# Optimization experiments

Hardware: AMD Instinct MI355X
Metric: run time of the kernel (lower is better)

The kernel has to match this reference:

```python
import jax, jax.numpy as jnp
import numpy as np

B, S, H = 128, 256, 512


def setup_inputs() -> dict:
    key = jax.random.key(0)
    ks = jax.random.split(key, 20)
    sc = 0.02
    inp = {
        "facts": jax.random.normal(ks[0], (B, S, H), jnp.float32),
        "questions": jax.random.normal(ks[1], (B, 1, H), jnp.float32),
        "prevM": jax.random.normal(ks[2], (B, 1, H), jnp.float32),
        # interaction gate MLP: z1 (4H->H), z2 (H->1)
        "z1_w": jax.random.normal(ks[3], (4 * H, H), jnp.float32) * sc,
        "z1_b": jnp.zeros((H,), jnp.float32),
        "z2_w": jax.random.normal(ks[4], (H, 1), jnp.float32) * sc,
        "z2_b": jnp.zeros((1,), jnp.float32),
        # AttentionGRUCell params (input_size = hidden_size = H)
        "Wr": jax.random.normal(ks[5], (H, H), jnp.float32) * sc,
        "br": jnp.zeros((H,), jnp.float32),
        "Ur": jax.random.normal(ks[6], (H, H), jnp.float32) * sc,
        "bur": jnp.zeros((H,), jnp.float32),
        "W": jax.random.normal(ks[7], (H, H), jnp.float32) * sc,
        "bw": jnp.zeros((H,), jnp.float32),
        "U": jax.random.normal(ks[8], (H, H), jnp.float32) * sc,
        "bu": jnp.zeros((H,), jnp.float32),
        # next memory projection (3H -> H)
        "nm_w": jax.random.normal(ks[9], (3 * H, H), jnp.float32) * sc,
        "nm_b": jnp.zeros((H,), jnp.float32),
    }
    return inp


def _episodic_memory(facts, questions, prevM,
                     z1_w, z1_b, z2_w, z2_b,
                     Wr, br, Ur, bur, W, bw, U, bu,
                     nm_w, nm_b):
    # ---- make_interaction ----
    q = questions  # (B,1,H) broadcasts against (B,S,H)
    m = prevM
    z = jnp.concatenate(
        [facts * q, facts * m, jnp.abs(facts - q), jnp.abs(facts - m)],
        axis=2,
    )  # (B,S,4H)
    g_hidden = jnp.tanh(jnp.einsum("bsf,fh->bsh", z, z1_w) + z1_b)
    G_logits = (jnp.einsum("bsh,ho->bso", g_hidden, z2_w) + z2_b)[..., 0]  # (B,S)
    G = jax.nn.softmax(G_logits, axis=1)  # (B,S)

    # ---- AttentionGRU scan over sentences ----
    pre_r = jnp.einsum("bsh,hk->bsh", facts, Wr) + br  # Wr @ fact, all steps
    pre_h = jnp.einsum("bsh,hk->bsh", facts, W) + bw   # W  @ fact, all steps

    def step(C, xs):
        pr, ph, g = xs  # (B,H), (B,H), (B,)
        r = jax.nn.sigmoid(pr + C @ Ur + bur)
        h_tilda = jnp.tanh(ph + r * (C @ U + bu))
        g = g[:, None]
        return g * h_tilda + (1.0 - g) * C, None

    C0 = jnp.zeros((facts.shape[0], Wr.shape[1]), facts.dtype)
    xs = (jnp.swapaxes(pre_r, 0, 1), jnp.swapaxes(pre_h, 0, 1), G.T)  # lead S
    C, _ = jax.lax.scan(step, C0, xs)  # (B,H)

    # ---- next memory ----
    concat = jnp.concatenate([prevM[:, 0], C, questions[:, 0]], axis=1)  # (B,3H)
    next_mem = jax.nn.relu(concat @ nm_w + nm_b)
    return next_mem[:, None, :]  # (B,1,H)


def reference(facts, questions, prevM, z1_w, z1_b, z2_w, z2_b,
              Wr, br, Ur, bur, W, bw, U, bu, nm_w, nm_b):
    return _episodic_memory(facts, questions, prevM, z1_w, z1_b, z2_w, z2_b,
                            Wr, br, Ur, bur, W, bw, U, bu, nm_w, nm_b)
```

## Files before the change

kernel.cpp:

```cpp
#include <hip/hip_runtime.h>
#include <stdint.h>

#define B_ 128
#define S_ 256
#define H_ 512

typedef __attribute__((ext_vector_type(4))) float f32x4;
typedef __attribute__((ext_vector_type(4))) int i32x4;
typedef __attribute__((ext_vector_type(2))) unsigned int u32x2;
typedef __attribute__((ext_vector_type(8))) __bf16 bf16x8;
typedef unsigned long long u64;

#define OFF_G      0
#define OFF_RSR    131072
#define OFF_RSH    133120
#define OFF_FLG    135168
#define OFF_EX     139264
#define OFF_CBUF   401408
#define OFF_BP     663552
#define OFF_PB     2760704
#define OFF_LOGITS 3809280

__device__ __forceinline__ unsigned short f2bf(float f) {
  unsigned u = __builtin_bit_cast(unsigned, f);
  u += 0x7FFFu + ((u >> 16) & 1u);
  return (unsigned short)(u >> 16);
}
__device__ __forceinline__ float fast_sigmoid(float x) {
  return 1.0f / (1.0f + __expf(-x));
}
__device__ __forceinline__ float fast_tanh(float x) {
  return 1.0f - 2.0f / (__expf(2.0f * x) + 1.0f);
}

__global__ void k_prep_bp(const float* __restrict__ z1w,
                          unsigned short* __restrict__ Bp) {
  int t = blockIdx.x * blockDim.x + threadIdx.x;
  int k = t >> 9, n = t & 511;
  Bp[((k >> 3) * 512 + n) * 8 + (k & 7)] = f2bf(z1w[t]);
}

__global__ void k_prep_pb(const float* __restrict__ Ur,
                          const float* __restrict__ U,
                          unsigned short* __restrict__ PB) {
  int t = blockIdx.x * blockDim.x + threadIdx.x;
  int j = t & 7;
  int l = (t >> 3) & 63;
  int kt = (t >> 9) & 15;
  int jn = (t >> 13) & 1;
  int w = (t >> 14) & 7;
  int mem = t >> 17;
  int k = kt * 32 + ((l >> 4) & 3) * 8 + j;
  int n = mem * 128 + ((w & 3) * 2 + jn) * 16 + (l & 15);
  const float* src = (w >> 2) ? U : Ur;
  PB[t] = f2bf(src[k * 512 + n]);
}

__global__ void k_prep_rs(const float* __restrict__ Wr,
                          const float* __restrict__ W,
                          float* __restrict__ rsr, float* __restrict__ rsh) {
  __shared__ float red[4];
  int h2 = blockIdx.x;
  int t = threadIdx.x;
  const float* M = (h2 >= 512) ? W : Wr;
  int h = h2 & 511;
  float sv = M[h * 512 + t] + M[h * 512 + 256 + t];
#pragma unroll
  for (int mask = 1; mask < 64; mask <<= 1) sv += __shfl_xor(sv, mask, 64);
  if ((t & 63) == 0) red[t >> 6] = sv;
  __syncthreads();
  if (t == 0) {
    float tot = red[0] + red[1] + red[2] + red[3];
    ((h2 >= 512) ? rsh : rsr)[h] = tot;
  }
}

__global__ __launch_bounds__(512, 4) void k_gate(
    const float* __restrict__ facts, const float* __restrict__ questions,
    const float* __restrict__ prevM, const float* __restrict__ z1b,
    const float* __restrict__ z2w, const unsigned short* __restrict__ Bp,
    float* __restrict__ logits) {
  __shared__ float qS[512], mS[512], z1bS[512], z2wS[512];
  __shared__ unsigned short At[64 * 40];
  __shared__ unsigned short Bt[16384];
  __shared__ float lp[64 * 4];
  const int tid = threadIdx.x;
  const int row0 = blockIdx.x * 64;
  const int b = row0 >> 8;
  const int s0 = row0 & 255;
  qS[tid] = questions[b * 512 + tid];
  mS[tid] = prevM[b * 512 + tid];
  z1bS[tid] = z1b[tid];
  z2wS[tid] = z2w[tid];
  const int w = tid >> 6, l = tid & 63;
  const int mgrp = w & 1, ngrp = w >> 1;
  const int lm = l & 15, lk = l >> 4;
  f32x4 acc[2][8];
#pragma unroll
  for (int a = 0; a < 2; ++a)
#pragma unroll
    for (int i = 0; i < 8; ++i) acc[a][i] = (f32x4){0.f, 0.f, 0.f, 0.f};
  const int arow = tid >> 3, ac = tid & 7;
  const float* fbase = facts + ((size_t)(b * 256 + s0 + arow)) * 512 + ac * 4;

  for (int kb = 0; kb < 64; ++kb) {
    __syncthreads();
    {
      const char* gsrc = (const char*)Bp + (size_t)kb * 32768 + w * 4096 + l * 16;
#pragma unroll
      for (int i = 0; i < 4; ++i)
        __builtin_amdgcn_global_load_lds(
            (const __attribute__((address_space(1))) unsigned int*)(gsrc +
                                                                    i * 1024),
            (__attribute__((address_space(3))) unsigned int*)((char*)Bt +
                                                              w * 4096 +
                                                              i * 1024),
            16, 0, 0);
    }
    const int part = kb >> 4;
    const int h0 = (kb & 15) * 32;
    f32x4 fv = *(const f32x4*)(fbase + h0);
    f32x4 ov = (part & 1) ? *(const f32x4*)&mS[h0 + ac * 4]
                          : *(const f32x4*)&qS[h0 + ac * 4];
    float z0, z1, z2, z3;
    if (part < 2) {
      z0 = fv[0] * ov[0]; z1 = fv[1] * ov[1];
      z2 = fv[2] * ov[2]; z3 = fv[3] * ov[3];
    } else {
      z0 = fabsf(fv[0] - ov[0]); z1 = fabsf(fv[1] - ov[1]);
      z2 = fabsf(fv[2] - ov[2]); z3 = fabsf(fv[3] - ov[3]);
    }
    unsigned p0 = (unsigned)f2bf(z0) | ((unsigned)f2bf(z1) << 16);
    unsigned p1 = (unsigned)f2bf(z2) | ((unsigned)f2bf(z3) << 16);
    u32x2 pk = {p0, p1};
    *(u32x2*)&At[arow * 40 + ac * 4] = pk;
    __syncthreads();
    bf16x8 af[2];
#pragma unroll
    for (int mi = 0; mi < 2; ++mi) {
      i32x4 av = *(const i32x4*)&At[((mgrp * 2 + mi) * 16 + lm) * 40 + lk * 8];
      af[mi] = __builtin_bit_cast(bf16x8, av);
    }
#pragma unroll
    for (int i = 0; i < 8; ++i) {
      const int nt = ngrp * 8 + i;
      i32x4 bv = *(const i32x4*)&Bt[lk * 4096 + (nt * 16 + lm) * 8];
      bf16x8 bf = __builtin_bit_cast(bf16x8, bv);
      acc[0][i] = __builtin_amdgcn_mfma_f32_16x16x32_bf16(af[0], bf, acc[0][i], 0, 0, 0);
      acc[1][i] = __builtin_amdgcn_mfma_f32_16x16x32_bf16(af[1], bf, acc[1][i], 0, 0, 0);
    }
  }
  float pr_[2][4];
#pragma unroll
  for (int mi = 0; mi < 2; ++mi)
#pragma unroll
    for (int r = 0; r < 4; ++r) pr_[mi][r] = 0.f;
#pragma unroll
  for (int i = 0; i < 8; ++i) {
    const int n_i = (ngrp * 8 + i) * 16 + lm;
    const float zb = z1bS[n_i], zw = z2wS[n_i];
#pragma unroll
    for (int mi = 0; mi < 2; ++mi)
#pragma unroll
      for (int r = 0; r < 4; ++r)
        pr_[mi][r] += fast_tanh(acc[mi][i][r] + zb) * zw;
  }
#pragma unroll
  for (int mask = 1; mask < 16; mask <<= 1)
#pragma unroll
    for (int mi = 0; mi < 2; ++mi)
#pragma unroll
      for (int r = 0; r < 4; ++r)
        pr_[mi][r] += __shfl_xor(pr_[mi][r], mask, 64);
  if (lm == 0) {
#pragma unroll
    for (int mi = 0; mi < 2; ++mi)
#pragma unroll
      for (int r = 0; r < 4; ++r)
        lp[((mgrp * 2 + mi) * 16 + lk * 4 + r) * 4 + ngrp] = pr_[mi][r];
  }
  __syncthreads();
  if (tid < 64)
    logits[row0 + tid] =
        lp[tid * 4] + lp[tid * 4 + 1] + lp[tid * 4 + 2] + lp[tid * 4 + 3];
}

__global__ void k_softmax(const float* __restrict__ logits,
                          float* __restrict__ G) {
  __shared__ float red[4], red2[4];
  int b = blockIdx.x, t = threadIdx.x;
  float v = logits[b * 256 + t];
  float mx = v;
#pragma unroll
  for (int mask = 1; mask < 64; mask <<= 1)
    mx = fmaxf(mx, __shfl_xor(mx, mask, 64));
  if ((t & 63) == 0) red[t >> 6] = mx;
  __syncthreads();
  mx = fmaxf(fmaxf(red[0], red[1]), fmaxf(red[2], red[3]));
  float e = __expf(v - mx);
  float sm = e;
#pragma unroll
  for (int mask = 1; mask < 64; mask <<= 1) sm += __shfl_xor(sm, mask, 64);
  if ((t & 63) == 0) red2[t >> 6] = sm;
  __syncthreads();
  sm = red2[0] + red2[1] + red2[2] + red2[3];
  G[b * 256 + t] = e / sm;
}

__global__ __launch_bounds__(512, 1) void k_scan(
    const float* __restrict__ facts, const float* __restrict__ Gm,
    const unsigned short* __restrict__ PB, const float* __restrict__ rsr,
    const float* __restrict__ rsh, const float* __restrict__ br,
    const float* __restrict__ bur, const float* __restrict__ bw,
    const float* __restrict__ bu, u64* __restrict__ EXq,
    unsigned int* __restrict__ FLG, float* __restrict__ Cb) {
  __shared__ unsigned short A[16 * 520];
  __shared__ float outb[16 * 272];
  const int tid = threadIdx.x;
  const int g = blockIdx.x & 7;
  const int mem = blockIdx.x >> 3;
  const int w = tid >> 6, l = tid & 63;
  const int lm = l & 15, lk = (l >> 4) & 3;
  for (int i = tid; i < 16 * 520 / 4; i += 512) ((u64*)A)[i] = 0ull;
  i32x4 bfr[2][16];
  const char* pb = (const char*)PB + (size_t)(mem * 8 + w) * 32768;
#pragma unroll
  for (int jn = 0; jn < 2; ++jn)
#pragma unroll
    for (int kt = 0; kt < 16; ++kt)
      bfr[jn][kt] = *(const i32x4*)(pb + (jn * 16 + kt) * 1024 + l * 16);
  const int ot = (w >> 2) * 8 + (w & 3) * 2;
  const int bb = tid >> 5;
  const int nqq = tid & 31;
  const int n0 = mem * 128 + nqq * 4;
  const int nl0 = nqq * 4;
  const int batch = g * 16 + bb;
  const f32x4 c_rsr = *(const f32x4*)(rsr + n0);
  const f32x4 c_br  = *(const f32x4*)(br + n0);
  const f32x4 c_rsh = *(const f32x4*)(rsh + n0);
  const f32x4 c_bw  = *(const f32x4*)(bw + n0);
  const f32x4 c_bur = *(const f32x4*)(bur + n0);
  const f32x4 c_bu  = *(const f32x4*)(bu + n0);
  const float* fptr = facts + (size_t)batch * 256 * 512 + n0;
  const float* gptr = Gm + batch * 256;
  const int grow = tid >> 5, gcu = tid & 31;
  const int pollmem = (tid < mem) ? tid : tid + 1;
  f32x4 Cv = (f32x4){0.f, 0.f, 0.f, 0.f};
  __syncthreads();

  for (int s = 0; s < 256; ++s) {
    const unsigned tag = (unsigned)(s + 1);
    const unsigned rbase = ((unsigned)(s & 1) * 8 + (unsigned)g) * 16;
    f32x4 fct = *(const f32x4*)(fptr + (size_t)s * 512);
    float gval = gptr[s];
    f32x4 acc0 = (f32x4){0.f, 0.f, 0.f, 0.f};
    f32x4 acc1 = (f32x4){0.f, 0.f, 0.f, 0.f};
#pragma unroll
    for (int kt = 0; kt < 16; ++kt) {
      i32x4 av = *(const i32x4*)&A[lm * 520 + kt * 32 + lk * 8];
      bf16x8 afv = __builtin_bit_cast(bf16x8, av);
      acc0 = __builtin_amdgcn_mfma_f32_16x16x32_bf16(
          afv, __builtin_bit_cast(bf16x8, bfr[0][kt]), acc0, 0, 0, 0);
      acc1 = __builtin_amdgcn_mfma_f32_16x16x32_bf16(
          afv, __builtin_bit_cast(bf16x8, bfr[1][kt]), acc1, 0, 0, 0);
    }
#pragma unroll
    for (int r = 0; r < 4; ++r) {
      outb[ot * 272 + (lk * 4 + r) * 17 + lm] = acc0[r];
      outb[(ot + 1) * 272 + (lk * 4 + r) * 17 + lm] = acc1[r];
    }
    __syncthreads();
    {
      unsigned short pk[4];
#pragma unroll
      for (int r = 0; r < 4; ++r) {
        const int n_loc = nl0 + r;
        const float uro = outb[(n_loc >> 4) * 272 + bb * 17 + (n_loc & 15)];
        const float uuo =
            outb[(8 + (n_loc >> 4)) * 272 + bb * 17 + (n_loc & 15)];
        const float pr = fct[r] * c_rsr[r] + c_br[r];
        const float ph = fct[r] * c_rsh[r] + c_bw[r];
        const float r_ = fast_sigmoid(pr + uro + c_bur[r]);
        const float ht = fast_tanh(ph + r_ * (uuo + c_bu[r]));
        Cv[r] = gval * ht + (1.0f - gval) * Cv[r];
        pk[r] = f2bf(Cv[r]);
      }
      const u64 word = (u64)pk[0] | ((u64)pk[1] << 16) | ((u64)pk[2] << 32) |
                       ((u64)pk[3] << 48);
      __hip_atomic_store(EXq + (rbase + (unsigned)bb) * 128 + (unsigned)(n0 >> 2),
                         word, __ATOMIC_RELAXED, __HIP_MEMORY_SCOPE_AGENT);
      *(u64*)((char*)A + bb * 1040 + n0 * 2) = word;
    }
    __syncthreads();
    if (tid == 0)
      __hip_atomic_store(FLG + g * 4 + mem, tag, __ATOMIC_RELAXED,
                         __HIP_MEMORY_SCOPE_AGENT);
    if (tid < 3) {
      int guard = 0;
      for (;;) {
        unsigned v = __hip_atomic_load(FLG + g * 4 + pollmem, __ATOMIC_RELAXED,
                                       __HIP_MEMORY_SCOPE_AGENT);
        if (v >= tag) break;
        __builtin_amdgcn_s_sleep(1);
        if (++guard > (1 << 22)) break;
      }
    }
    __syncthreads();
#pragma unroll
    for (int q = 0; q < 4; ++q) {
      if (q != mem) {
        u64 wv = __hip_atomic_load(
            EXq + (rbase + (unsigned)grow) * 128 + (unsigned)(q * 32 + gcu),
            __ATOMIC_RELAXED, __HIP_MEMORY_SCOPE_AGENT);
        *(u64*)((char*)A + grow * 1040 + q * 256 + gcu * 8) = wv;
      }
    }
    __syncthreads();
  }
  *(f32x4*)(Cb + (size_t)batch * 512 + n0) = Cv;
}

__global__ __launch_bounds__(512) void k_final(
    const float* __restrict__ prevM, const float* __restrict__ questions,
    const float* __restrict__ Cb, const float* __restrict__ nmw,
    const float* __restrict__ nmb, float* __restrict__ out) {
  __shared__ float cc[2][1536];
  const int t = threadIdx.x;
  const int b0 = blockIdx.x * 2;
  for (int i = t; i < 1536; i += 512) {
#pragma unroll
    for (int bi = 0; bi < 2; ++bi) {
      int bbx = b0 + bi;
      float v;
      if (i < 512) v = prevM[bbx * 512 + i];
      else if (i < 1024) v = Cb[bbx * 512 + i - 512];
      else v = questions[bbx * 512 + i - 1024];
      cc[bi][i] = v;
    }
  }
  __syncthreads();
  const int h = t;
  float a0 = nmb[h], a1 = nmb[h];
#pragma unroll 4
  for (int f = 0; f < 1536; ++f) {
    float wv = nmw[f * 512 + h];
    a0 = fmaf(cc[0][f], wv, a0);
    a1 = fmaf(cc[1][f], wv, a1);
  }
  out[(size_t)b0 * 512 + h] = fmaxf(a0, 0.f);
  out[(size_t)(b0 + 1) * 512 + h] = fmaxf(a1, 0.f);
}

extern "C" void kernel_launch(void* const* d_in, const int* in_sizes, int n_in,
                              void* d_out, int out_size, void* d_ws,
                              size_t ws_size, hipStream_t stream) {
  const float* facts     = (const float*)d_in[0];
  const float* questions = (const float*)d_in[1];
  const float* prevM     = (const float*)d_in[2];
  const float* z1w       = (const float*)d_in[3];
  const float* z1b       = (const float*)d_in[4];
  const float* z2w       = (const float*)d_in[5];
  const float* Wr        = (const float*)d_in[7];
  const float* br        = (const float*)d_in[8];
  const float* Ur        = (const float*)d_in[9];
  const float* bur       = (const float*)d_in[10];
  const float* W         = (const float*)d_in[11];
  const float* bw        = (const float*)d_in[12];
  const float* U         = (const float*)d_in[13];
  const float* bu        = (const float*)d_in[14];
  const float* nmw       = (const float*)d_in[15];
  const float* nmb       = (const float*)d_in[16];

  char* ws = (char*)d_ws;
  float* G             = (float*)(ws + OFF_G);
  float* rsr           = (float*)(ws + OFF_RSR);
  float* rsh           = (float*)(ws + OFF_RSH);
  unsigned* FLG        = (unsigned*)(ws + OFF_FLG);
  u64* EXq             = (u64*)(ws + OFF_EX);
  float* Cb            = (float*)(ws + OFF_CBUF);
  float* logits        = (float*)(ws + OFF_LOGITS);
  unsigned short* Bp   = (unsigned short*)(ws + OFF_BP);
  unsigned short* PB   = (unsigned short*)(ws + OFF_PB);

  hipMemsetAsync(FLG, 0, 32 * sizeof(unsigned), stream);
  k_prep_bp<<<2048, 512, 0, stream>>>(z1w, Bp);
  k_prep_pb<<<1024, 512, 0, stream>>>(Ur, U, PB);
  k_prep_rs<<<1024, 256, 0, stream>>>(Wr, W, rsr, rsh);
  k_gate<<<512, 512, 0, stream>>>(facts, questions, prevM, z1b, z2w, Bp, logits);
  k_softmax<<<128, 256, 0, stream>>>(logits, G);
  k_scan<<<32, 512, 0, stream>>>(facts, G, PB, rsr, rsh, br, bur, bw, bu, EXq,
                                 FLG, Cb);
  k_final<<<64, 512, 0, stream>>>(prevM, questions, Cb, nmw, nmb, (float*)d_out);
}
```

Before: 1.140 ms.

## Compute GRU gates directly in MFMA accumulator layout and prefetch next-step inputs

Reorders the packed Ur/U weight layout so each wave's two MFMA accumulators hold the Ur and U products for the same 16 output columns. The gate math can then run directly on accumulator registers, removing the LDS round-trip through outb and one barrier per step. Facts and gate values for the next step are prefetched during the current step, using a transposed G written by softmax. Flag polling is spread across all threads, and the exchange loads are batched. The cost is more scattered 4-byte global stores of packed bf16 pairs built with shuffles.

```diff
diff --git a/kernel.cpp b/kernel.cpp
--- a/kernel.cpp
+++ b/kernel.cpp
@@ -47,12 +47,12 @@
   int j = t & 7;
   int l = (t >> 3) & 63;
   int kt = (t >> 9) & 15;
-  int jn = (t >> 13) & 1;
+  int mat = (t >> 13) & 1;
   int w = (t >> 14) & 7;
   int mem = t >> 17;
   int k = kt * 32 + ((l >> 4) & 3) * 8 + j;
-  int n = mem * 128 + ((w & 3) * 2 + jn) * 16 + (l & 15);
-  const float* src = (w >> 2) ? U : Ur;
+  int n = mem * 128 + w * 16 + (l & 15);
+  const float* src = mat ? U : Ur;
   PB[t] = f2bf(src[k * 512 + n]);
 }
 
@@ -186,7 +186,7 @@
 }
 
 __global__ void k_softmax(const float* __restrict__ logits,
-                          float* __restrict__ G) {
+                          float* __restrict__ GT) {
   __shared__ float red[4], red2[4];
   int b = blockIdx.x, t = threadIdx.x;
   float v = logits[b * 256 + t];
@@ -204,18 +204,17 @@
   if ((t & 63) == 0) red2[t >> 6] = sm;
   __syncthreads();
   sm = red2[0] + red2[1] + red2[2] + red2[3];
-  G[b * 256 + t] = e / sm;
+  GT[t * 128 + b] = e / sm;
 }
 
 __global__ __launch_bounds__(512, 1) void k_scan(
-    const float* __restrict__ facts, const float* __restrict__ Gm,
+    const float* __restrict__ facts, const float* __restrict__ GT,
     const unsigned short* __restrict__ PB, const float* __restrict__ rsr,
     const float* __restrict__ rsh, const float* __restrict__ br,
     const float* __restrict__ bur, const float* __restrict__ bw,
-    const float* __restrict__ bu, u64* __restrict__ EXq,
+    const float* __restrict__ bu, unsigned int* __restrict__ EX,
     unsigned int* __restrict__ FLG, float* __restrict__ Cb) {
   __shared__ unsigned short A[16 * 520];
-  __shared__ float outb[16 * 272];
   const int tid = threadIdx.x;
   const int g = blockIdx.x & 7;
   const int mem = blockIdx.x >> 3;
@@ -225,34 +224,31 @@
   i32x4 bfr[2][16];
   const char* pb = (const char*)PB + (size_t)(mem * 8 + w) * 32768;
 #pragma unroll
-  for (int jn = 0; jn < 2; ++jn)
+  for (int mat = 0; mat < 2; ++mat)
 #pragma unroll
     for (int kt = 0; kt < 16; ++kt)
-      bfr[jn][kt] = *(const i32x4*)(pb + (jn * 16 + kt) * 1024 + l * 16);
-  const int ot = (w >> 2) * 8 + (w & 3) * 2;
-  const int bb = tid >> 5;
-  const int nqq = tid & 31;
-  const int n0 = mem * 128 + nqq * 4;
-  const int nl0 = nqq * 4;
-  const int batch = g * 16 + bb;
-  const f32x4 c_rsr = *(const f32x4*)(rsr + n0);
-  const f32x4 c_br  = *(const f32x4*)(br + n0);
-  const f32x4 c_rsh = *(const f32x4*)(rsh + n0);
-  const f32x4 c_bw  = *(const f32x4*)(bw + n0);
-  const f32x4 c_bur = *(const f32x4*)(bur + n0);
-  const f32x4 c_bu  = *(const f32x4*)(bu + n0);
-  const float* fptr = facts + (size_t)batch * 256 * 512 + n0;
-  const float* gptr = Gm + batch * 256;
+      bfr[mat][kt] = *(const i32x4*)(pb + (mat * 16 + kt) * 1024 + l * 16);
+  const int n = mem * 128 + w * 16 + lm;
+  const int b0 = g * 16 + lk * 4;
+  const float c_rsr = rsr[n], c_br = br[n];
+  const float c_rsh = rsh[n], c_bw = bw[n];
+  const float c_bur = bur[n], c_bu = bu[n];
+  const float* fb[4];
+#pragma unroll
+  for (int r = 0; r < 4; ++r)
+    fb[r] = facts + (size_t)(b0 + r) * (256 * 512) + n;
   const int grow = tid >> 5, gcu = tid & 31;
-  const int pollmem = (tid < mem) ? tid : tid + 1;
+  const u64* EXQ = (const u64*)EX;
   f32x4 Cv = (f32x4){0.f, 0.f, 0.f, 0.f};
+  float fct[4];
+#pragma unroll
+  for (int r = 0; r < 4; ++r) fct[r] = fb[r][0];
+  f32x4 gvv = *(const f32x4*)(GT + b0);
   __syncthreads();
 
   for (int s = 0; s < 256; ++s) {
     const unsigned tag = (unsigned)(s + 1);
     const unsigned rbase = ((unsigned)(s & 1) * 8 + (unsigned)g) * 16;
-    f32x4 fct = *(const f32x4*)(fptr + (size_t)s * 512);
-    float gval = gptr[s];
     f32x4 acc0 = (f32x4){0.f, 0.f, 0.f, 0.f};
     f32x4 acc1 = (f32x4){0.f, 0.f, 0.f, 0.f};
 #pragma unroll
@@ -264,60 +260,75 @@
       acc1 = __builtin_amdgcn_mfma_f32_16x16x32_bf16(
           afv, __builtin_bit_cast(bf16x8, bfr[1][kt]), acc1, 0, 0, 0);
     }
+    unsigned pkd[4];
 #pragma unroll
     for (int r = 0; r < 4; ++r) {
-      outb[ot * 272 + (lk * 4 + r) * 17 + lm] = acc0[r];
-      outb[(ot + 1) * 272 + (lk * 4 + r) * 17 + lm] = acc1[r];
-    }
-    __syncthreads();
-    {
-      unsigned short pk[4];
-#pragma unroll
-      for (int r = 0; r < 4; ++r) {
-        const int n_loc = nl0 + r;
-        const float uro = outb[(n_loc >> 4) * 272 + bb * 17 + (n_loc & 15)];
-        const float uuo =
-            outb[(8 + (n_loc >> 4)) * 272 + bb * 17 + (n_loc & 15)];
-        const float pr = fct[r] * c_rsr[r] + c_br[r];
-        const float ph = fct[r] * c_rsh[r] + c_bw[r];
-        const float r_ = fast_sigmoid(pr + uro + c_bur[r]);
-        const float ht = fast_tanh(ph + r_ * (uuo + c_bu[r]));
-        Cv[r] = gval * ht + (1.0f - gval) * Cv[r];
-        pk[r] = f2bf(Cv[r]);
-      }
-      const u64 word = (u64)pk[0] | ((u64)pk[1] << 16) | ((u64)pk[2] << 32) |
-                       ((u64)pk[3] << 48);
-      __hip_atomic_store(EXq + (rbase + (unsigned)bb) * 128 + (unsigned)(n0 >> 2),
-                         word, __ATOMIC_RELAXED, __HIP_MEMORY_SCOPE_AGENT);
-      *(u64*)((char*)A + bb * 1040 + n0 * 2) = word;
+      const float pr = fct[r] * c_rsr + c_br;
+      const float ph = fct[r] * c_rsh + c_bw;
+      const float r_ = fast_sigmoid(pr + acc0[r] + c_bur);
+      const float ht = fast_tanh(ph + r_ * (acc1[r] + c_bu));
+      Cv[r] = gvv[r] * ht + (1.0f - gvv[r]) * Cv[r];
+      const int mb = (int)f2bf(Cv[r]);
+      pkd[r] = (unsigned)mb | ((unsigned)__shfl_xor(mb, 1, 64) << 16);
+    }
+    if (!(lm & 1)) {
+#pragma unroll
+      for (int r = 0; r < 4; ++r)
+        __hip_atomic_store(EX + (rbase + (unsigned)(lk * 4 + r)) * 256 +
+                               ((unsigned)n >> 1),
+                           pkd[r], __ATOMIC_RELAXED, __HIP_MEMORY_SCOPE_AGENT);
+    }
+    float fctn[4];
+    f32x4 gvn = gvv;
+    if (s < 255) {
+#pragma unroll
+      for (int r = 0; r < 4; ++r) fctn[r] = fb[r][(size_t)(s + 1) * 512];
+      gvn = *(const f32x4*)(GT + (s + 1) * 128 + b0);
+    } else {
+#pragma unroll
+      for (int r = 0; r < 4; ++r) fctn[r] = 0.f;
     }
     __syncthreads();
     if (tid == 0)
       __hip_atomic_store(FLG + g * 4 + mem, tag, __ATOMIC_RELAXED,
                          __HIP_MEMORY_SCOPE_AGENT);
-    if (tid < 3) {
-      int guard = 0;
-      for (;;) {
-        unsigned v = __hip_atomic_load(FLG + g * 4 + pollmem, __ATOMIC_RELAXED,
-                                       __HIP_MEMORY_SCOPE_AGENT);
-        if (v >= tag) break;
-        __builtin_amdgcn_s_sleep(1);
-        if (++guard > (1 << 22)) break;
+    if (!(lm & 1)) {
+#pragma unroll
+      for (int r = 0; r < 4; ++r)
+        *(unsigned*)((char*)A + (lk * 4 + r) * 1040 + n * 2) = pkd[r];
+    }
+    {
+#pragma unroll
+      for (int j = 0; j < 3; ++j) {
+        const int q = j + (j >= mem ? 1 : 0);
+        int guard = 0;
+        while (__hip_atomic_load(FLG + g * 4 + q, __ATOMIC_RELAXED,
+                                 __HIP_MEMORY_SCOPE_AGENT) < tag) {
+          __builtin_amdgcn_s_sleep(1);
+          if (++guard > (1 << 22)) break;
+        }
       }
+      u64 wv[3];
+#pragma unroll
+      for (int j = 0; j < 3; ++j) {
+        const int q = j + (j >= mem ? 1 : 0);
+        wv[j] = __hip_atomic_load(
+            EXQ + (rbase + (unsigned)grow) * 128 + (unsigned)(q * 32 + gcu),
+            __ATOMIC_RELAXED, __HIP_MEMORY_SCOPE_AGENT);
+      }
+#pragma unroll
+      for (int j = 0; j < 3; ++j) {
+        const int q = j + (j >= mem ? 1 : 0);
+        *(u64*)((char*)A + grow * 1040 + q * 256 + gcu * 8) = wv[j];
+      }
     }
     __syncthreads();
 #pragma unroll
-    for (int q = 0; q < 4; ++q) {
-      if (q != mem) {
-        u64 wv = __hip_atomic_load(
-            EXq + (rbase + (unsigned)grow) * 128 + (unsigned)(q * 32 + gcu),
-            __ATOMIC_RELAXED, __HIP_MEMORY_SCOPE_AGENT);
-        *(u64*)((char*)A + grow * 1040 + q * 256 + gcu * 8) = wv;
-      }
-    }
-    __syncthreads();
-  }
-  *(f32x4*)(Cb + (size_t)batch * 512 + n0) = Cv;
+    for (int r = 0; r < 4; ++r) fct[r] = fctn[r];
+    gvv = gvn;
+  }
+#pragma unroll
+  for (int r = 0; r < 4; ++r) Cb[(size_t)(b0 + r) * 512 + n] = Cv[r];
 }
 
 __global__ __launch_bounds__(512) void k_final(
@@ -372,11 +383,11 @@
   const float* nmb       = (const float*)d_in[16];
 
   char* ws = (char*)d_ws;
-  float* G             = (float*)(ws + OFF_G);
+  float* GT            = (float*)(ws + OFF_G);
   float* rsr           = (float*)(ws + OFF_RSR);
   float* rsh           = (float*)(ws + OFF_RSH);
   unsigned* FLG        = (unsigned*)(ws + OFF_FLG);
-  u64* EXq             = (u64*)(ws + OFF_EX);
+  unsigned* EX         = (unsigned*)(ws + OFF_EX);
   float* Cb            = (float*)(ws + OFF_CBUF);
   float* logits        = (float*)(ws + OFF_LOGITS);
   unsigned short* Bp   = (unsigned short*)(ws + OFF_BP);
@@ -387,8 +398,8 @@
   k_prep_pb<<<1024, 512, 0, stream>>>(Ur, U, PB);
   k_prep_rs<<<1024, 256, 0, stream>>>(Wr, W, rsr, rsh);
   k_gate<<<512, 512, 0, stream>>>(facts, questions, prevM, z1b, z2w, Bp, logits);
-  k_softmax<<<128, 256, 0, stream>>>(logits, G);
-  k_scan<<<32, 512, 0, stream>>>(facts, G, PB, rsr, rsh, br, bur, bw, bu, EXq,
+  k_softmax<<<128, 256, 0, stream>>>(logits, GT);
+  k_scan<<<32, 512, 0, stream>>>(facts, GT, PB, rsr, rsh, br, bur, bw, bu, EX,
                                  FLG, Cb);
   k_final<<<64, 512, 0, stream>>>(prevM, questions, Cb, nmw, nmb, (float*)d_out);
 }
```

Result: no change. 1.121 ms (-1.6%).
